# Performance work log

Hardware: AMD Instinct MI355X
Metric: run time of the kernel (lower is better)

The kernel has to match this reference:

```python
import jax, jax.numpy as jnp
import numpy as np

V, E, HN, HH, D, T, B = 10000, 512, 1024, 256, 4, 128, 64


def setup_inputs() -> dict:
    key = jax.random.key(0)
    ks = jax.random.split(key, 9)
    s = lambda k, shape: jax.random.normal(k, shape, jnp.float32) * 0.02
    return {
        "x": jax.random.randint(ks[0], (B, T), 0, V),
        "embed": s(ks[1], (V, E)),
        "Whh": s(ks[2], (2 * HH, HH)), "bhh": jnp.zeros((2 * HH,), jnp.float32),
        "Wih": s(ks[3], (2 * HH, E)), "bih": jnp.zeros((2 * HH,), jnp.float32),
        "Wh": s(ks[4], (2 * HN, HN)), "bh": jnp.zeros((2 * HN,), jnp.float32),
        "Wi": s(ks[5], (2 * HN, E)), "bi": jnp.zeros((2 * HN,), jnp.float32),
        "Wup": s(ks[6], (HN, HH)), "bup": jnp.zeros((HN,), jnp.float32),
        "Wout": s(ks[7], (V, HN)), "bout": jnp.zeros((V,), jnp.float32),
    }


def _gate(Ws, s):
    # highwayGate: split into carry/transform halves (eval mode: no gate dropout)
    hh, tt = jnp.split(Ws, 2, axis=1)
    tt = jax.nn.sigmoid(tt)
    return jnp.tanh(hh) * tt + s * (1.0 - tt)


def reference(x, embed, Whh, bhh, Wih, bih, Wh, bh, Wi, bi, Wup, bup, Wout, bout):
    emb = embed[x]                      # [B, T, E]
    xs = jnp.swapaxes(emb, 0, 1)        # [T, B, E] for scan over time

    def step(carry, xt):
        sH, sN = carry
        for i in range(D):  # depth: weights SHARED across all i (ModuleList(depth*[m]))
            Ws = sH @ Whh.T + bhh
            if i == 0:
                Ws = Ws + xt @ Wih.T + bih
            sH = _gate(Ws, sH)
            z = sH @ Wup.T + bup        # [B, HN]
            zz = jnp.concatenate([z, z], axis=1)  # scale both gate halves
            Ws = (sN @ Wh.T + bh) * zz  # HyperLinear: row-scaled linear
            if i == 0:
                Ws = Ws + (xt @ Wi.T + bi) * zz
            sN = _gate(Ws, sN)
        return (sH, sN), sN

    init = (jnp.zeros((B, HH), jnp.float32), jnp.zeros((B, HN), jnp.float32))
    _, outs = jax.lax.scan(step, init, xs)   # outs: [T, B, HN]
    h = jnp.swapaxes(outs, 0, 1)             # [B, T, HN]
    return h @ Wout.T + bout                 # [B, T, V]
```

## Files before the change

kernel.cpp:

```cpp
#include <hip/hip_runtime.h>
#include <hip/hip_cooperative_groups.h>

namespace cg = cooperative_groups;

typedef float v2f __attribute__((ext_vector_type(2)));

#define B_  64
#define T_  128
#define E_  512
#define HH_ 256
#define HN_ 1024
#define D_  4
#define V_  10000
#define NR_ (T_*D_)
#define NWG_ 256

#define WH_STR   1032
#define WI_STR   520
#define WS_STR   264
#define WH_OFF   0
#define WU_OFF   8256
#define WI_OFF   9312
#define WHH_OFF  13472
#define WIH_OFF  21920
#define LDS_FLOATS 38560

__device__ __forceinline__ void flag_barrier(int* __restrict__ flags,
                                             int* __restrict__ gen,
                                             int w, int tau, int target)
{
    __syncthreads();
    if (tau == 0) {
        __builtin_amdgcn_fence(__ATOMIC_RELEASE, "agent");
        __hip_atomic_store(&flags[w * 16], target, __ATOMIC_RELAXED,
                           __HIP_MEMORY_SCOPE_AGENT);
    }
    if (w == 0) {
        if (tau < NWG_) {
            while (__hip_atomic_load(&flags[tau * 16], __ATOMIC_RELAXED,
                                     __HIP_MEMORY_SCOPE_AGENT) < target) {
                __builtin_amdgcn_s_sleep(1);
            }
        }
        __syncthreads();
        if (tau == 0)
            __hip_atomic_store(gen, target, __ATOMIC_RELAXED,
                               __HIP_MEMORY_SCOPE_AGENT);
    } else if (tau == 0) {
        while (__hip_atomic_load(gen, __ATOMIC_RELAXED,
                                 __HIP_MEMORY_SCOPE_AGENT) < target) {
            __builtin_amdgcn_s_sleep(1);
        }
    }
    if (tau == 0)
        __builtin_amdgcn_fence(__ATOMIC_ACQUIRE, "agent");
    __syncthreads();
}

__global__ __launch_bounds__(1024, 1) void recur_kernel(
    const int*   __restrict__ xx,
    const float* __restrict__ embed,
    const float* __restrict__ Whh, const float* __restrict__ bhh,
    const float* __restrict__ Wih, const float* __restrict__ bih,
    const float* __restrict__ Wh,  const float* __restrict__ bh,
    const float* __restrict__ Wi,  const float* __restrict__ bi,
    const float* __restrict__ Wup, const float* __restrict__ bup,
    float* __restrict__ sH,
    float* __restrict__ sN,
    float* __restrict__ hOut,
    int*   __restrict__ flags,
    int*   __restrict__ gen)
{
    extern __shared__ float lds[];
    cg::grid_group grid = cg::this_grid();
    const int w   = blockIdx.x;
    const int tau = threadIdx.x;
    const int gid = w * 1024 + tau;
    const int ch0 = (w & 15) * 16;

    for (int idx = tau; idx < 2048; idx += 1024) {
        int r = idx >> 8, kq = idx & 255;
        int grow = w*4 + (r & 3) + (r >> 2) * HN_;
        *(float4*)&lds[WH_OFF + r*WH_STR + kq*4] =
            *(const float4*)(Wh + (size_t)grow * HN_ + kq*4);
    }
    if (tau < 256) {
        int r = tau >> 6, kq = tau & 63;
        *(float4*)&lds[WU_OFF + r*WS_STR + kq*4] =
            *(const float4*)(Wup + (size_t)(w*4 + r) * HH_ + kq*4);
    }
    if (tau < 1024) {
        int r = tau >> 7, kq = tau & 127;
        int grow = w*4 + (r & 3) + (r >> 2) * HN_;
        *(float4*)&lds[WI_OFF + r*WI_STR + kq*4] =
            *(const float4*)(Wi + (size_t)grow * E_ + kq*4);
    }
    for (int idx = tau; idx < 2048; idx += 1024) {
        int r = idx >> 6, kq = idx & 63;
        int grow = ch0 + (r & 15) + (r >> 4) * HH_;
        *(float4*)&lds[WHH_OFF + r*WS_STR + kq*4] =
            *(const float4*)(Whh + (size_t)grow * HH_ + kq*4);
    }
    for (int idx = tau; idx < 4096; idx += 1024) {
        int r = idx >> 7, kq = idx & 127;
        int grow = ch0 + (r & 15) + (r >> 4) * HH_;
        *(float4*)&lds[WIH_OFF + r*WI_STR + kq*4] =
            *(const float4*)(Wih + (size_t)grow * E_ + kq*4);
    }

    if (gid < B_ * HH_) sH[gid] = 0.f;
    if (gid < B_ * HN_) sN[B_ * HN_ + gid] = 0.f;
    if (tau == 0) flags[w * 16] = 0;
    if (w == 0 && tau == 0) *gen = 0;
    __syncthreads();
    grid.sync();

    const int kk = tau & 3;
    const int jj = (tau >> 2) & 3;
    const int b  = tau >> 4;
    const int j  = w * 4 + jj;
    const float bh1 = bh[j],  bh2 = bh[j + HN_];
    const float bi1 = bi[j],  bi2 = bi[j + HN_];
    const float bupj = bup[j];
    const float* wr1 = lds + WH_OFF + jj * WH_STR + kk * 4;
    const float* wr2 = lds + WH_OFF + (4 + jj) * WH_STR + kk * 4;
    const float* yr1 = lds + WI_OFF + jj * WI_STR + kk * 4;
    const float* yr2 = lds + WI_OFF + (4 + jj) * WI_STR + kk * 4;
    const float* ur  = lds + WU_OFF + jj * WS_STR + kk * 4;

    const bool hduty = (tau & 3) == 3;
    const int kkh  = (tau >> 2) & 3;
    const int item = tau >> 4;
    const int ch   = ch0 + (item & 15);
    const int bH   = (w >> 4) * 4 + (item >> 4);
    const float bhh1 = bhh[ch], bhh2 = bhh[ch + HH_];
    const float bih1 = bih[ch], bih2 = bih[ch + HH_];
    const float* q1 = lds + WHH_OFF + (ch & 15) * WS_STR + kkh * 4;
    const float* q2 = lds + WHH_OFF + (16 + (ch & 15)) * WS_STR + kkh * 4;
    const float* p1 = lds + WIH_OFF + (ch & 15) * WI_STR + kkh * 4;
    const float* p2 = lds + WIH_OFF + (16 + (ch & 15)) * WI_STR + kkh * 4;

    for (int r = 0; r <= NR_; ++r) {
        const int p = r & 1;
        const float* sNp = sN + p * (B_ * HN_);
        const float* sHp = sH + p * (B_ * HH_);
        float* sNn = sN + (1 - p) * (B_ * HN_);
        float* sHn = sH + (1 - p) * (B_ * HH_);

        if (r >= 1) {
            const int s = r - 1;
            const int t = s >> 2;
            const int i = s & 3;

            v2f acc1 = {0.f, 0.f}, acc2 = {0.f, 0.f};
            const float4* sv = (const float4*)(sNp + b * HN_);
            for (int kc = 0; kc < 64; kc += 8) {
                float4 sreg[8];
                #pragma unroll
                for (int u = 0; u < 8; ++u) sreg[u] = sv[kk + 4*(kc + u)];
                #pragma unroll
                for (int u = 0; u < 8; ++u) {
                    float4 a  = sreg[u];
                    float4 x1 = *(const float4*)(wr1 + (kc + u) * 16);
                    float4 x2 = *(const float4*)(wr2 + (kc + u) * 16);
                    v2f a0 = {a.x, a.y},   a1v = {a.z, a.w};
                    v2f w10 = {x1.x, x1.y}, w11 = {x1.z, x1.w};
                    v2f w20 = {x2.x, x2.y}, w21 = {x2.z, x2.w};
                    acc1 += a0 * w10;  acc1 += a1v * w11;
                    acc2 += a0 * w20;  acc2 += a1v * w21;
                }
            }
            if (i == 0) {
                const int tok = xx[b * T_ + t];
                const float4* ev = (const float4*)(embed + (size_t)tok * E_);
                for (int kc = 0; kc < 32; kc += 8) {
                    float4 sreg[8];
                    #pragma unroll
                    for (int u = 0; u < 8; ++u) sreg[u] = ev[kk + 4*(kc + u)];
                    #pragma unroll
                    for (int u = 0; u < 8; ++u) {
                        float4 a  = sreg[u];
                        float4 x1 = *(const float4*)(yr1 + (kc + u) * 16);
                        float4 x2 = *(const float4*)(yr2 + (kc + u) * 16);
                        v2f a0 = {a.x, a.y},   a1v = {a.z, a.w};
                        v2f w10 = {x1.x, x1.y}, w11 = {x1.z, x1.w};
                        v2f w20 = {x2.x, x2.y}, w21 = {x2.z, x2.w};
                        acc1 += a0 * w10;  acc1 += a1v * w11;
                        acc2 += a0 * w20;  acc2 += a1v * w21;
                    }
                }
            }
            v2f zacc = {0.f, 0.f};
            {
                const float4* hv = (const float4*)(sHp + b * HH_);
                float4 sreg[8];
                #pragma unroll
                for (int u = 0; u < 8; ++u) sreg[u] = hv[kk + 4*u];
                #pragma unroll
                for (int u = 0; u < 8; ++u) {
                    float4 a  = sreg[u];
                    float4 x1 = *(const float4*)(ur + u * 16);
                    v2f a0 = {a.x, a.y},   a1v = {a.z, a.w};
                    v2f w10 = {x1.x, x1.y}, w11 = {x1.z, x1.w};
                    zacc += a0 * w10;  zacc += a1v * w11;
                }
                #pragma unroll
                for (int u = 8; u < 16; ++u) sreg[u-8] = hv[kk + 4*u];
                #pragma unroll
                for (int u = 8; u < 16; ++u) {
                    float4 a  = sreg[u-8];
                    float4 x1 = *(const float4*)(ur + u * 16);
                    v2f a0 = {a.x, a.y},   a1v = {a.z, a.w};
                    v2f w10 = {x1.x, x1.y}, w11 = {x1.z, x1.w};
                    zacc += a0 * w10;  zacc += a1v * w11;
                }
            }
            float A1 = acc1.x + acc1.y;
            float A2 = acc2.x + acc2.y;
            float Z  = zacc.x + zacc.y;
            A1 += __shfl_xor(A1, 1); A1 += __shfl_xor(A1, 2);
            A2 += __shfl_xor(A2, 1); A2 += __shfl_xor(A2, 2);
            Z  += __shfl_xor(Z, 1);  Z  += __shfl_xor(Z, 2);
            if (kk == 0) {
                float g1 = A1 + bh1, g2 = A2 + bh2;
                if (i == 0) { g1 += bi1; g2 += bi2; }
                const float zv  = Z + bupj;
                const float g_h = g1 * zv;
                const float g_t = g2 * zv;
                const float sg  = 1.f / (1.f + expf(-g_t));
                const float ov  = sNp[b * HN_ + j];
                const float nv  = tanhf(g_h) * sg + ov * (1.f - sg);
                sNn[b * HN_ + j] = nv;
                if (i == D_ - 1) hOut[(size_t)(b * T_ + t) * HN_ + j] = nv;
            }
        }

        if (r < NR_ && hduty) {
            const int t = r >> 2;
            const int i = r & 3;
            v2f A = {0.f, 0.f}, Bv = {0.f, 0.f};
            const float4* svh = (const float4*)(sHp + bH * HH_);
            {
                float4 sreg[8];
                #pragma unroll
                for (int u = 0; u < 8; ++u) sreg[u] = svh[kkh + 4*u];
                #pragma unroll
                for (int u = 0; u < 8; ++u) {
                    float4 a  = sreg[u];
                    float4 x1 = *(const float4*)(q1 + u * 16);
                    float4 x2 = *(const float4*)(q2 + u * 16);
                    v2f a0 = {a.x, a.y},   a1v = {a.z, a.w};
                    v2f w10 = {x1.x, x1.y}, w11 = {x1.z, x1.w};
                    v2f w20 = {x2.x, x2.y}, w21 = {x2.z, x2.w};
                    A  += a0 * w10;  A  += a1v * w11;
                    Bv += a0 * w20;  Bv += a1v * w21;
                }
                #pragma unroll
                for (int u = 8; u < 16; ++u) sreg[u-8] = svh[kkh + 4*u];
                #pragma unroll
                for (int u = 8; u < 16; ++u) {
                    float4 a  = sreg[u-8];
                    float4 x1 = *(const float4*)(q1 + u * 16);
                    float4 x2 = *(const float4*)(q2 + u * 16);
                    v2f a0 = {a.x, a.y},   a1v = {a.z, a.w};
                    v2f w10 = {x1.x, x1.y}, w11 = {x1.z, x1.w};
                    v2f w20 = {x2.x, x2.y}, w21 = {x2.z, x2.w};
                    A  += a0 * w10;  A  += a1v * w11;
                    Bv += a0 * w20;  Bv += a1v * w21;
                }
            }
            if (i == 0) {
                const int tok = xx[bH * T_ + t];
                const float4* ev = (const float4*)(embed + (size_t)tok * E_);
                for (int kc = 0; kc < 32; kc += 8) {
                    float4 sreg[8];
                    #pragma unroll
                    for (int u = 0; u < 8; ++u) sreg[u] = ev[kkh + 4*(kc + u)];
                    #pragma unroll
                    for (int u = 0; u < 8; ++u) {
                        float4 a  = sreg[u];
                        float4 x1 = *(const float4*)(p1 + (kc + u) * 16);
                        float4 x2 = *(const float4*)(p2 + (kc + u) * 16);
                        v2f a0 = {a.x, a.y},   a1v = {a.z, a.w};
                        v2f w10 = {x1.x, x1.y}, w11 = {x1.z, x1.w};
                        v2f w20 = {x2.x, x2.y}, w21 = {x2.z, x2.w};
                        A  += a0 * w10;  A  += a1v * w11;
                        Bv += a0 * w20;  Bv += a1v * w21;
                    }
                }
            }
            float a1 = A.x + A.y;
            float a2 = Bv.x + Bv.y;
            a1 += __shfl_xor(a1, 4); a1 += __shfl_xor(a1, 8);
            a2 += __shfl_xor(a2, 4); a2 += __shfl_xor(a2, 8);
            if (kkh == 0) {
                a1 += bhh1; a2 += bhh2;
                if (i == 0) { a1 += bih1; a2 += bih2; }
                const float sg = 1.f / (1.f + expf(-a2));
                const float ov = sHp[bH * HH_ + ch];
                sHn[bH * HH_ + ch] = tanhf(a1) * sg + ov * (1.f - sg);
            }
        }

        flag_barrier(flags, gen, w, tau, r + 1);
    }
}

__global__ __launch_bounds__(256) void out_gemm(
    const float* __restrict__ hb, const float* __restrict__ Wout,
    const float* __restrict__ bout, float* __restrict__ op)
{
    __shared__ float Ht[32][64];
    __shared__ float Wt[32][64];
    const int tau = threadIdx.x;
    const int tx  = tau & 15;
    const int ty  = tau >> 4;
    const int m0  = blockIdx.x * 64;
    const int n0  = blockIdx.y * 64;
    float acc[4][4] = {{0.f}};

    for (int k0 = 0; k0 < HN_; k0 += 32) {
        #pragma unroll
        for (int l = 0; l < 2; ++l) {
            const int f   = tau + l * 256;
            const int row = f >> 3;
            const int kq  = (f & 7) * 4;
            float4 hv = *(const float4*)(hb + (size_t)(m0 + row) * HN_ + k0 + kq);
            Ht[kq + 0][row] = hv.x; Ht[kq + 1][row] = hv.y;
            Ht[kq + 2][row] = hv.z; Ht[kq + 3][row] = hv.w;
            const int vr = n0 + row;
            float4 wv = (vr < V_) ? *(const float4*)(Wout + (size_t)vr * HN_ + k0 + kq)
                                  : make_float4(0.f, 0.f, 0.f, 0.f);
            Wt[kq + 0][row] = wv.x; Wt[kq + 1][row] = wv.y;
            Wt[kq + 2][row] = wv.z; Wt[kq + 3][row] = wv.w;
        }
        __syncthreads();
        #pragma unroll
        for (int kk = 0; kk < 32; ++kk) {
            float4 av = *(const float4*)(&Ht[kk][ty * 4]);
            float4 bv = *(const float4*)(&Wt[kk][tx * 4]);
            acc[0][0] += av.x * bv.x; acc[0][1] += av.x * bv.y;
            acc[0][2] += av.x * bv.z; acc[0][3] += av.x * bv.w;
            acc[1][0] += av.y * bv.x; acc[1][1] += av.y * bv.y;
            acc[1][2] += av.y * bv.z; acc[1][3] += av.y * bv.w;
            acc[2][0] += av.z * bv.x; acc[2][1] += av.z * bv.y;
            acc[2][2] += av.z * bv.z; acc[2][3] += av.z * bv.w;
            acc[3][0] += av.w * bv.x; acc[3][1] += av.w * bv.y;
            acc[3][2] += av.w * bv.z; acc[3][3] += av.w * bv.w;
        }
        __syncthreads();
    }

    #pragma unroll
    for (int ii = 0; ii < 4; ++ii) {
        const int m = m0 + ty * 4 + ii;
        #pragma unroll
        for (int jq = 0; jq < 4; ++jq) {
            const int v = n0 + tx * 4 + jq;
            if (v < V_) op[(size_t)m * V_ + v] = acc[ii][jq] + bout[v];
        }
    }
}

extern "C" void kernel_launch(void* const* d_in, const int* in_sizes, int n_in,
                              void* d_out, int out_size, void* d_ws, size_t ws_size,
                              hipStream_t stream) {
    const int*   xx    = (const int*)  d_in[0];
    const float* embed = (const float*)d_in[1];
    const float* Whh   = (const float*)d_in[2];
    const float* bhh   = (const float*)d_in[3];
    const float* Wih   = (const float*)d_in[4];
    const float* bih   = (const float*)d_in[5];
    const float* Wh    = (const float*)d_in[6];
    const float* bh    = (const float*)d_in[7];
    const float* Wi    = (const float*)d_in[8];
    const float* bi    = (const float*)d_in[9];
    const float* Wup   = (const float*)d_in[10];
    const float* bup   = (const float*)d_in[11];
    const float* Wout  = (const float*)d_in[12];
    const float* bout  = (const float*)d_in[13];

    float* ws   = (float*)d_ws;
    float* hbuf = ws;
    float* sHb  = hbuf + (size_t)B_ * T_ * HN_;
    float* sNb  = sHb + 2 * B_ * HH_;
    int*   flg  = (int*)(sNb + 2 * B_ * HN_);
    int*   gen  = flg + NWG_ * 16;

    void* args[] = { (void*)&xx, (void*)&embed, (void*)&Whh, (void*)&bhh,
                     (void*)&Wih, (void*)&bih, (void*)&Wh, (void*)&bh,
                     (void*)&Wi, (void*)&bi, (void*)&Wup, (void*)&bup,
                     (void*)&sHb, (void*)&sNb, (void*)&hbuf,
                     (void*)&flg, (void*)&gen };
    hipLaunchCooperativeKernel(reinterpret_cast<void*>(recur_kernel),
                               dim3(256), dim3(1024), args,
                               (size_t)(LDS_FLOATS * 4), stream);

    out_gemm<<<dim3(T_ * B_ / 64, (V_ + 63) / 64), 256, 0, stream>>>(
        hbuf, Wout, bout, (float*)d_out);
}
```

Measured before the change: 15.26 ms.

## Remap recurrent-step threads to 4 batches per lane with DPP row reductions

Reorganizes the per-step work mapping in the persistent recurrent kernel: each thread now handles four batch rows with 16-way K splits, reusing each LDS weight load across four state vectors instead of one. Reductions use DPP row-sum instructions instead of shuffles, and the small sH gate is computed by all threads with rotated LDS access instead of only a quarter of them. This aims to cut LDS weight traffic and idle lanes on the serial critical path, at the cost of more registers and select logic for writeback.

```diff
diff --git a/kernel.cpp b/kernel.cpp
--- a/kernel.cpp
+++ b/kernel.cpp
@@ -24,6 +24,22 @@
 #define WHH_OFF  13472
 #define WIH_OFF  21920
 #define LDS_FLOATS 38560
+
+__device__ __forceinline__ float row16_sum(float x) {
+    int v = __builtin_bit_cast(int, x);
+    x += __builtin_bit_cast(float, __builtin_amdgcn_update_dpp(0, v, 0xB1, 0xF, 0xF, true));
+    v = __builtin_bit_cast(int, x);
+    x += __builtin_bit_cast(float, __builtin_amdgcn_update_dpp(0, v, 0x4E, 0xF, 0xF, true));
+    v = __builtin_bit_cast(int, x);
+    x += __builtin_bit_cast(float, __builtin_amdgcn_update_dpp(0, v, 0x124, 0xF, 0xF, true));
+    v = __builtin_bit_cast(int, x);
+    x += __builtin_bit_cast(float, __builtin_amdgcn_update_dpp(0, v, 0x128, 0xF, 0xF, true));
+    return x;
+}
+
+__device__ __forceinline__ float sel4(int s, float a, float b, float c, float d) {
+    return s == 0 ? a : (s == 1 ? b : (s == 2 ? c : d));
+}
 
 __device__ __forceinline__ void flag_barrier(int* __restrict__ flags,
                                              int* __restrict__ gen,
@@ -115,30 +131,29 @@
     __syncthreads();
     grid.sync();
 
-    const int kk = tau & 3;
-    const int jj = (tau >> 2) & 3;
-    const int b  = tau >> 4;
-    const int j  = w * 4 + jj;
+    const int lane = tau & 63;
+    const int bq   = tau >> 6;
+    const int kk   = lane & 15;
+    const int jj   = lane >> 4;
+
+    const int j = w * 4 + jj;
     const float bh1 = bh[j],  bh2 = bh[j + HN_];
     const float bi1 = bi[j],  bi2 = bi[j + HN_];
     const float bupj = bup[j];
-    const float* wr1 = lds + WH_OFF + jj * WH_STR + kk * 4;
-    const float* wr2 = lds + WH_OFF + (4 + jj) * WH_STR + kk * 4;
-    const float* yr1 = lds + WI_OFF + jj * WI_STR + kk * 4;
-    const float* yr2 = lds + WI_OFF + (4 + jj) * WI_STR + kk * 4;
-    const float* ur  = lds + WU_OFF + jj * WS_STR + kk * 4;
-
-    const bool hduty = (tau & 3) == 3;
-    const int kkh  = (tau >> 2) & 3;
-    const int item = tau >> 4;
-    const int ch   = ch0 + (item & 15);
-    const int bH   = (w >> 4) * 4 + (item >> 4);
+    const float* wrow1 = lds + WH_OFF + jj * WH_STR;
+    const float* wrow2 = lds + WH_OFF + (4 + jj) * WH_STR;
+    const float* urow  = lds + WU_OFF + jj * WS_STR;
+    const float* yrow1 = lds + WI_OFF + jj * WI_STR;
+    const float* yrow2 = lds + WI_OFF + (4 + jj) * WI_STR;
+
+    const int ch = ch0 + bq;
+    const int bH = (w >> 4) * 4 + jj;
     const float bhh1 = bhh[ch], bhh2 = bhh[ch + HH_];
     const float bih1 = bih[ch], bih2 = bih[ch + HH_];
-    const float* q1 = lds + WHH_OFF + (ch & 15) * WS_STR + kkh * 4;
-    const float* q2 = lds + WHH_OFF + (16 + (ch & 15)) * WS_STR + kkh * 4;
-    const float* p1 = lds + WIH_OFF + (ch & 15) * WI_STR + kkh * 4;
-    const float* p2 = lds + WIH_OFF + (16 + (ch & 15)) * WI_STR + kkh * 4;
+    const float* qrow1 = lds + WHH_OFF + bq * WS_STR;
+    const float* qrow2 = lds + WHH_OFF + (16 + bq) * WS_STR;
+    const float* prow1 = lds + WIH_OFF + bq * WI_STR;
+    const float* prow2 = lds + WIH_OFF + (16 + bq) * WI_STR;
 
     for (int r = 0; r <= NR_; ++r) {
         const int p = r & 1;
@@ -152,153 +167,169 @@
             const int t = s >> 2;
             const int i = s & 3;
 
-            v2f acc1 = {0.f, 0.f}, acc2 = {0.f, 0.f};
-            const float4* sv = (const float4*)(sNp + b * HN_);
-            for (int kc = 0; kc < 64; kc += 8) {
-                float4 sreg[8];
-                #pragma unroll
-                for (int u = 0; u < 8; ++u) sreg[u] = sv[kk + 4*(kc + u)];
+            const float* sb0 = sNp + (bq * 4 + 0) * HN_;
+            const float* sb1 = sNp + (bq * 4 + 1) * HN_;
+            const float* sb2 = sNp + (bq * 4 + 2) * HN_;
+            const float* sb3 = sNp + (bq * 4 + 3) * HN_;
+
+            v2f A1[4], A2[4], Z[4];
+            #pragma unroll
+            for (int bb = 0; bb < 4; ++bb) { A1[bb] = (v2f){0.f,0.f}; A2[bb] = (v2f){0.f,0.f}; Z[bb] = (v2f){0.f,0.f}; }
+
+            #pragma unroll
+            for (int u = 0; u < 16; ++u) {
+                const int fi = (u * 16 + kk) * 4;
+                float4 w1 = *(const float4*)(wrow1 + fi);
+                float4 w2 = *(const float4*)(wrow2 + fi);
+                float4 s0 = *(const float4*)(sb0 + fi);
+                float4 s1 = *(const float4*)(sb1 + fi);
+                float4 s2 = *(const float4*)(sb2 + fi);
+                float4 s3 = *(const float4*)(sb3 + fi);
+                v2f w1l = {w1.x, w1.y}, w1h = {w1.z, w1.w};
+                v2f w2l = {w2.x, w2.y}, w2h = {w2.z, w2.w};
+                v2f a;
+                a = (v2f){s0.x, s0.y}; A1[0] += a * w1l; A2[0] += a * w2l;
+                a = (v2f){s0.z, s0.w}; A1[0] += a * w1h; A2[0] += a * w2h;
+                a = (v2f){s1.x, s1.y}; A1[1] += a * w1l; A2[1] += a * w2l;
+                a = (v2f){s1.z, s1.w}; A1[1] += a * w1h; A2[1] += a * w2h;
+                a = (v2f){s2.x, s2.y}; A1[2] += a * w1l; A2[2] += a * w2l;
+                a = (v2f){s2.z, s2.w}; A1[2] += a * w1h; A2[2] += a * w2h;
+                a = (v2f){s3.x, s3.y}; A1[3] += a * w1l; A2[3] += a * w2l;
+                a = (v2f){s3.z, s3.w}; A1[3] += a * w1h; A2[3] += a * w2h;
+            }
+
+            if (i == 0) {
+                const int t0 = xx[(bq * 4 + 0) * T_ + t];
+                const int t1 = xx[(bq * 4 + 1) * T_ + t];
+                const int t2 = xx[(bq * 4 + 2) * T_ + t];
+                const int t3 = xx[(bq * 4 + 3) * T_ + t];
+                const float* e0 = embed + (size_t)t0 * E_;
+                const float* e1 = embed + (size_t)t1 * E_;
+                const float* e2 = embed + (size_t)t2 * E_;
+                const float* e3 = embed + (size_t)t3 * E_;
                 #pragma unroll
                 for (int u = 0; u < 8; ++u) {
-                    float4 a  = sreg[u];
-                    float4 x1 = *(const float4*)(wr1 + (kc + u) * 16);
-                    float4 x2 = *(const float4*)(wr2 + (kc + u) * 16);
-                    v2f a0 = {a.x, a.y},   a1v = {a.z, a.w};
-                    v2f w10 = {x1.x, x1.y}, w11 = {x1.z, x1.w};
-                    v2f w20 = {x2.x, x2.y}, w21 = {x2.z, x2.w};
-                    acc1 += a0 * w10;  acc1 += a1v * w11;
-                    acc2 += a0 * w20;  acc2 += a1v * w21;
+                    const int fi = (u * 16 + kk) * 4;
+                    float4 y1 = *(const float4*)(yrow1 + fi);
+                    float4 y2 = *(const float4*)(yrow2 + fi);
+                    float4 v0 = *(const float4*)(e0 + fi);
+                    float4 v1 = *(const float4*)(e1 + fi);
+                    float4 v2 = *(const float4*)(e2 + fi);
+                    float4 v3 = *(const float4*)(e3 + fi);
+                    v2f y1l = {y1.x, y1.y}, y1h = {y1.z, y1.w};
+                    v2f y2l = {y2.x, y2.y}, y2h = {y2.z, y2.w};
+                    v2f a;
+                    a = (v2f){v0.x, v0.y}; A1[0] += a * y1l; A2[0] += a * y2l;
+                    a = (v2f){v0.z, v0.w}; A1[0] += a * y1h; A2[0] += a * y2h;
+                    a = (v2f){v1.x, v1.y}; A1[1] += a * y1l; A2[1] += a * y2l;
+                    a = (v2f){v1.z, v1.w}; A1[1] += a * y1h; A2[1] += a * y2h;
+                    a = (v2f){v2.x, v2.y}; A1[2] += a * y1l; A2[2] += a * y2l;
+                    a = (v2f){v2.z, v2.w}; A1[2] += a * y1h; A2[2] += a * y2h;
+                    a = (v2f){v3.x, v3.y}; A1[3] += a * y1l; A2[3] += a * y2l;
+                    a = (v2f){v3.z, v3.w}; A1[3] += a * y1h; A2[3] += a * y2h;
                 }
             }
-            if (i == 0) {
-                const int tok = xx[b * T_ + t];
-                const float4* ev = (const float4*)(embed + (size_t)tok * E_);
-                for (int kc = 0; kc < 32; kc += 8) {
-                    float4 sreg[8];
-                    #pragma unroll
-                    for (int u = 0; u < 8; ++u) sreg[u] = ev[kk + 4*(kc + u)];
-                    #pragma unroll
-                    for (int u = 0; u < 8; ++u) {
-                        float4 a  = sreg[u];
-                        float4 x1 = *(const float4*)(yr1 + (kc + u) * 16);
-                        float4 x2 = *(const float4*)(yr2 + (kc + u) * 16);
-                        v2f a0 = {a.x, a.y},   a1v = {a.z, a.w};
-                        v2f w10 = {x1.x, x1.y}, w11 = {x1.z, x1.w};
-                        v2f w20 = {x2.x, x2.y}, w21 = {x2.z, x2.w};
-                        acc1 += a0 * w10;  acc1 += a1v * w11;
-                        acc2 += a0 * w20;  acc2 += a1v * w21;
-                    }
+
+            {
+                const float* hb0 = sHp + (bq * 4 + 0) * HH_;
+                const float* hb1 = sHp + (bq * 4 + 1) * HH_;
+                const float* hb2 = sHp + (bq * 4 + 2) * HH_;
+                const float* hb3 = sHp + (bq * 4 + 3) * HH_;
+                #pragma unroll
+                for (int u = 0; u < 4; ++u) {
+                    const int fi = (u * 16 + kk) * 4;
+                    float4 uw = *(const float4*)(urow + fi);
+                    float4 h0 = *(const float4*)(hb0 + fi);
+                    float4 h1 = *(const float4*)(hb1 + fi);
+                    float4 h2 = *(const float4*)(hb2 + fi);
+                    float4 h3 = *(const float4*)(hb3 + fi);
+                    v2f ul = {uw.x, uw.y}, uh = {uw.z, uw.w};
+                    v2f a;
+                    a = (v2f){h0.x, h0.y}; Z[0] += a * ul;
+                    a = (v2f){h0.z, h0.w}; Z[0] += a * uh;
+                    a = (v2f){h1.x, h1.y}; Z[1] += a * ul;
+                    a = (v2f){h1.z, h1.w}; Z[1] += a * uh;
+                    a = (v2f){h2.x, h2.y}; Z[2] += a * ul;
+                    a = (v2f){h2.z, h2.w}; Z[2] += a * uh;
+                    a = (v2f){h3.x, h3.y}; Z[3] += a * ul;
+                    a = (v2f){h3.z, h3.w}; Z[3] += a * uh;
                 }
             }
-            v2f zacc = {0.f, 0.f};
-            {
-                const float4* hv = (const float4*)(sHp + b * HH_);
-                float4 sreg[8];
-                #pragma unroll
-                for (int u = 0; u < 8; ++u) sreg[u] = hv[kk + 4*u];
-                #pragma unroll
-                for (int u = 0; u < 8; ++u) {
-                    float4 a  = sreg[u];
-                    float4 x1 = *(const float4*)(ur + u * 16);
-                    v2f a0 = {a.x, a.y},   a1v = {a.z, a.w};
-                    v2f w10 = {x1.x, x1.y}, w11 = {x1.z, x1.w};
-                    zacc += a0 * w10;  zacc += a1v * w11;
-                }
-                #pragma unroll
-                for (int u = 8; u < 16; ++u) sreg[u-8] = hv[kk + 4*u];
-                #pragma unroll
-                for (int u = 8; u < 16; ++u) {
-                    float4 a  = sreg[u-8];
-                    float4 x1 = *(const float4*)(ur + u * 16);
-                    v2f a0 = {a.x, a.y},   a1v = {a.z, a.w};
-                    v2f w10 = {x1.x, x1.y}, w11 = {x1.z, x1.w};
-                    zacc += a0 * w10;  zacc += a1v * w11;
-                }
-            }
-            float A1 = acc1.x + acc1.y;
-            float A2 = acc2.x + acc2.y;
-            float Z  = zacc.x + zacc.y;
-            A1 += __shfl_xor(A1, 1); A1 += __shfl_xor(A1, 2);
-            A2 += __shfl_xor(A2, 1); A2 += __shfl_xor(A2, 2);
-            Z  += __shfl_xor(Z, 1);  Z  += __shfl_xor(Z, 2);
-            if (kk == 0) {
-                float g1 = A1 + bh1, g2 = A2 + bh2;
+
+            float a1r0 = row16_sum(A1[0].x + A1[0].y);
+            float a1r1 = row16_sum(A1[1].x + A1[1].y);
+            float a1r2 = row16_sum(A1[2].x + A1[2].y);
+            float a1r3 = row16_sum(A1[3].x + A1[3].y);
+            float a2r0 = row16_sum(A2[0].x + A2[0].y);
+            float a2r1 = row16_sum(A2[1].x + A2[1].y);
+            float a2r2 = row16_sum(A2[2].x + A2[2].y);
+            float a2r3 = row16_sum(A2[3].x + A2[3].y);
+            float zr0  = row16_sum(Z[0].x + Z[0].y);
+            float zr1  = row16_sum(Z[1].x + Z[1].y);
+            float zr2  = row16_sum(Z[2].x + Z[2].y);
+            float zr3  = row16_sum(Z[3].x + Z[3].y);
+
+            const int bsel = bq * 4 + (kk & 3);
+            const float ov = sNp[bsel * HN_ + j];
+
+            if (kk < 4) {
+                float g1 = sel4(kk, a1r0, a1r1, a1r2, a1r3) + bh1;
+                float g2 = sel4(kk, a2r0, a2r1, a2r2, a2r3) + bh2;
                 if (i == 0) { g1 += bi1; g2 += bi2; }
-                const float zv  = Z + bupj;
+                const float zv  = sel4(kk, zr0, zr1, zr2, zr3) + bupj;
                 const float g_h = g1 * zv;
                 const float g_t = g2 * zv;
                 const float sg  = 1.f / (1.f + expf(-g_t));
-                const float ov  = sNp[b * HN_ + j];
                 const float nv  = tanhf(g_h) * sg + ov * (1.f - sg);
-                sNn[b * HN_ + j] = nv;
-                if (i == D_ - 1) hOut[(size_t)(b * T_ + t) * HN_ + j] = nv;
-            }
-        }
-
-        if (r < NR_ && hduty) {
+                sNn[bsel * HN_ + j] = nv;
+                if (i == D_ - 1) hOut[(size_t)(bsel * T_ + t) * HN_ + j] = nv;
+            }
+        }
+
+        if (r < NR_) {
             const int t = r >> 2;
             const int i = r & 3;
-            v2f A = {0.f, 0.f}, Bv = {0.f, 0.f};
-            const float4* svh = (const float4*)(sHp + bH * HH_);
-            {
-                float4 sreg[8];
-                #pragma unroll
-                for (int u = 0; u < 8; ++u) sreg[u] = svh[kkh + 4*u];
-                #pragma unroll
-                for (int u = 0; u < 8; ++u) {
-                    float4 a  = sreg[u];
-                    float4 x1 = *(const float4*)(q1 + u * 16);
-                    float4 x2 = *(const float4*)(q2 + u * 16);
-                    v2f a0 = {a.x, a.y},   a1v = {a.z, a.w};
-                    v2f w10 = {x1.x, x1.y}, w11 = {x1.z, x1.w};
-                    v2f w20 = {x2.x, x2.y}, w21 = {x2.z, x2.w};
-                    A  += a0 * w10;  A  += a1v * w11;
-                    Bv += a0 * w20;  Bv += a1v * w21;
-                }
-                #pragma unroll
-                for (int u = 8; u < 16; ++u) sreg[u-8] = svh[kkh + 4*u];
-                #pragma unroll
-                for (int u = 8; u < 16; ++u) {
-                    float4 a  = sreg[u-8];
-                    float4 x1 = *(const float4*)(q1 + u * 16);
-                    float4 x2 = *(const float4*)(q2 + u * 16);
-                    v2f a0 = {a.x, a.y},   a1v = {a.z, a.w};
-                    v2f w10 = {x1.x, x1.y}, w11 = {x1.z, x1.w};
-                    v2f w20 = {x2.x, x2.y}, w21 = {x2.z, x2.w};
-                    A  += a0 * w10;  A  += a1v * w11;
-                    Bv += a0 * w20;  Bv += a1v * w21;
-                }
+            v2f a1v = {0.f, 0.f}, a2v = {0.f, 0.f};
+            const float* shb = sHp + bH * HH_;
+            #pragma unroll
+            for (int uu = 0; uu < 4; ++uu) {
+                const int fi = (((jj + uu) & 3) * 16 + kk) * 4;
+                float4 q1 = *(const float4*)(qrow1 + fi);
+                float4 q2 = *(const float4*)(qrow2 + fi);
+                float4 sv = *(const float4*)(shb + fi);
+                v2f q1l = {q1.x, q1.y}, q1h = {q1.z, q1.w};
+                v2f q2l = {q2.x, q2.y}, q2h = {q2.z, q2.w};
+                v2f a;
+                a = (v2f){sv.x, sv.y}; a1v += a * q1l; a2v += a * q2l;
+                a = (v2f){sv.z, sv.w}; a1v += a * q1h; a2v += a * q2h;
             }
             if (i == 0) {
                 const int tok = xx[bH * T_ + t];
-                const float4* ev = (const float4*)(embed + (size_t)tok * E_);
-                for (int kc = 0; kc < 32; kc += 8) {
-                    float4 sreg[8];
-                    #pragma unroll
-                    for (int u = 0; u < 8; ++u) sreg[u] = ev[kkh + 4*(kc + u)];
-                    #pragma unroll
-                    for (int u = 0; u < 8; ++u) {
-                        float4 a  = sreg[u];
-                        float4 x1 = *(const float4*)(p1 + (kc + u) * 16);
-                        float4 x2 = *(const float4*)(p2 + (kc + u) * 16);
-                        v2f a0 = {a.x, a.y},   a1v = {a.z, a.w};
-                        v2f w10 = {x1.x, x1.y}, w11 = {x1.z, x1.w};
-                        v2f w20 = {x2.x, x2.y}, w21 = {x2.z, x2.w};
-                        A  += a0 * w10;  A  += a1v * w11;
-                        Bv += a0 * w20;  Bv += a1v * w21;
-                    }
+                const float* eb = embed + (size_t)tok * E_;
+                #pragma unroll
+                for (int uu = 0; uu < 4; ++uu) {
+                    const int fi = (((jj + uu) & 3) * 16 + kk) * 4;
+                    float4 p1a = *(const float4*)(prow1 + fi);
+                    float4 p1b = *(const float4*)(prow1 + fi + 256);
+                    float4 p2a = *(const float4*)(prow2 + fi);
+                    float4 p2b = *(const float4*)(prow2 + fi + 256);
+                    float4 ea  = *(const float4*)(eb + fi);
+                    float4 eb2 = *(const float4*)(eb + fi + 256);
+                    v2f a;
+                    a = (v2f){ea.x, ea.y};  a1v += a * (v2f){p1a.x, p1a.y}; a2v += a * (v2f){p2a.x, p2a.y};
+                    a = (v2f){ea.z, ea.w};  a1v += a * (v2f){p1a.z, p1a.w}; a2v += a * (v2f){p2a.z, p2a.w};
+                    a = (v2f){eb2.x, eb2.y}; a1v += a * (v2f){p1b.x, p1b.y}; a2v += a * (v2f){p2b.x, p2b.y};
+                    a = (v2f){eb2.z, eb2.w}; a1v += a * (v2f){p1b.z, p1b.w}; a2v += a * (v2f){p2b.z, p2b.w};
                 }
             }
-            float a1 = A.x + A.y;
-            float a2 = Bv.x + Bv.y;
-            a1 += __shfl_xor(a1, 4); a1 += __shfl_xor(a1, 8);
-            a2 += __shfl_xor(a2, 4); a2 += __shfl_xor(a2, 8);
-            if (kkh == 0) {
+            float a1 = row16_sum(a1v.x + a1v.y);
+            float a2 = row16_sum(a2v.x + a2v.y);
+            const float ovh = sHp[bH * HH_ + ch];
+            if (kk == 0) {
                 a1 += bhh1; a2 += bhh2;
                 if (i == 0) { a1 += bih1; a2 += bih2; }
                 const float sg = 1.f / (1.f + expf(-a2));
-                const float ov = sHp[bH * HH_ + ch];
-                sHn[bH * HH_ + ch] = tanhf(a1) * sg + ov * (1.f - sg);
+                sHn[bH * HH_ + ch] = tanhf(a1) * sg + ovh * (1.f - sg);
             }
         }
 
@@ -336,9 +367,9 @@
         }
         __syncthreads();
         #pragma unroll
-        for (int kk = 0; kk < 32; ++kk) {
-            float4 av = *(const float4*)(&Ht[kk][ty * 4]);
-            float4 bv = *(const float4*)(&Wt[kk][tx * 4]);
+        for (int kq = 0; kq < 32; ++kq) {
+            float4 av = *(const float4*)(&Ht[kq][ty * 4]);
+            float4 bv = *(const float4*)(&Wt[kq][tx * 4]);
             acc[0][0] += av.x * bv.x; acc[0][1] += av.x * bv.y;
             acc[0][2] += av.x * bv.z; acc[0][3] += av.x * bv.w;
             acc[1][0] += av.y * bv.x; acc[1][1] += av.y * bv.y;
```

New measurement: 13.29 ms. 12.9% less time.
